# Performance work log

Measured on AMD Instinct MI355X. Metric: run time of the kernel, lower is better.

## Reference

```python
import jax, jax.numpy as jnp
import numpy as np

N_NODES = 100000
D_IN = 256
D_HID = 64
D_EMB = 32
ADJ_NNZ = 3200000
N_EDGES = 2000000


def setup_inputs() -> dict:
    key = jax.random.key(0)
    ks = jax.random.split(key, 8)
    x = jax.random.normal(ks[0], (N_NODES, D_IN), dtype=jnp.float32)
    adj_src = jax.random.randint(ks[1], (ADJ_NNZ,), 0, N_NODES, dtype=jnp.int32)
    adj_dst = jax.random.randint(ks[2], (ADJ_NNZ,), 0, N_NODES, dtype=jnp.int32)
    adj_val = jax.random.uniform(ks[3], (ADJ_NNZ,), dtype=jnp.float32)
    edge_index = jax.random.randint(ks[4], (2, N_EDGES), 0, N_NODES, dtype=jnp.int32)
    # Xavier-uniform weights, zero biases (matches reset_parameters)
    lim1 = float(np.sqrt(6.0 / (D_IN + D_HID)))
    lim2 = float(np.sqrt(6.0 / (D_HID + D_EMB)))
    W1 = jax.random.uniform(ks[5], (D_IN, D_HID), minval=-lim1, maxval=lim1, dtype=jnp.float32)
    b1 = jnp.zeros((D_HID,), dtype=jnp.float32)
    W2 = jax.random.uniform(ks[6], (D_HID, D_EMB), minval=-lim2, maxval=lim2, dtype=jnp.float32)
    b2 = jnp.zeros((D_EMB,), dtype=jnp.float32)
    return {"x": x, "adj_src": adj_src, "adj_dst": adj_dst, "adj_val": adj_val,
            "edge_index": edge_index, "W1": W1, "b1": b1, "W2": W2, "b2": b2}


def _spmm(adj_src, adj_dst, adj_val, dense):
    # (sparse A) @ dense : out[i] = sum_{e: dst[e]==i} val[e] * dense[src[e]]
    n = dense.shape[0]
    msgs = adj_val[:, None] * dense[adj_src]            # [nnz, d]
    return jax.ops.segment_sum(msgs, adj_dst, num_segments=n)


def reference(x, adj_src, adj_dst, adj_val, edge_index, W1, b1, W2, b2):
    # Layer 1: ReLU(A_norm @ (x W1) + b1)
    z1 = jax.nn.relu(_spmm(adj_src, adj_dst, adj_val, x @ W1) + b1)
    # Layer 2: A_norm @ (z1 W2) + b2 (no activation)
    z2 = _spmm(adj_src, adj_dst, adj_val, z1 @ W2) + b2   # [n, d_emb]
    # Inner-product decoder over edges
    src, dst = edge_index[0], edge_index[1]
    scores = jnp.sum(z2[src] * z2[dst], axis=1)          # [num_edges]
    return scores
```

## Files before the change

### kernel.cpp

```cpp
#include <hip/hip_runtime.h>
#include <hip/hip_bf16.h>


#define D_IN  256
#define D_HID 64
#define D_EMB 32
#define BROWS 256
#define NBUK_MAX 512
#define TILE  4096
#define PBS   512
#define SBS   1024

typedef unsigned char u8;
typedef unsigned short u16;
typedef unsigned int u32;
typedef __attribute__((ext_vector_type(8))) short short8;
typedef __attribute__((ext_vector_type(4))) float f32x4;
typedef __attribute__((ext_vector_type(2))) float f32x2;

__device__ __forceinline__ float bf2f(u32 u) {
  return __uint_as_float((u & 0xFFFFu) << 16);
}
__device__ __forceinline__ float bf2f_hi(u32 u) {
  return __uint_as_float(u & 0xFFFF0000u);
}
__device__ __forceinline__ u16 f2bf(float f) {
  u32 x = __float_as_uint(f);
  x += 0x7FFFu + ((x >> 16) & 1u);
  return (u16)(x >> 16);
}
__device__ __forceinline__ void unpack8(uint4 u, float* f) {
  f[0] = bf2f(u.x); f[1] = bf2f(u.x >> 16);
  f[2] = bf2f(u.y); f[3] = bf2f(u.y >> 16);
  f[4] = bf2f(u.z); f[5] = bf2f(u.z >> 16);
  f[6] = bf2f(u.w); f[7] = bf2f(u.w >> 16);
}

__global__ __launch_bounds__(256) void w1_swizzle_kernel(
    const float* __restrict__ W1, uint4* __restrict__ gswz) {
  const int s = blockIdx.x * 256 + threadIdx.x;
  const int lane = s & 63;
  const int kstep = (s >> 6) & 7;
  const int nt = s >> 9;
  const int col = nt * 16 + (lane & 15);
  const int kbase = kstep * 32 + (lane >> 4) * 8;
  u32 p[4];
  for (int jp = 0; jp < 4; ++jp) {
    u32 lo = f2bf(W1[(kbase + 2 * jp) * D_HID + col]);
    u32 hi = f2bf(W1[(kbase + 2 * jp + 1) * D_HID + col]);
    p[jp] = lo | (hi << 16);
  }
  gswz[s] = make_uint4(p[0], p[1], p[2], p[3]);
}

__global__ __launch_bounds__(256) void bin_count(
    const int* __restrict__ dst, int* __restrict__ hist, int nnz, int nbuk) {
  __shared__ int h[NBUK_MAX];
  for (int i = threadIdx.x; i < nbuk; i += 256) h[i] = 0;
  __syncthreads();
  const int stride = gridDim.x * 256;
  for (int e = blockIdx.x * 256 + threadIdx.x; e < nnz; e += stride)
    atomicAdd(&h[dst[e] >> 8], 1);
  __syncthreads();
  for (int i = threadIdx.x; i < nbuk; i += 256) {
    int v = h[i];
    if (v) atomicAdd(&hist[i], v);
  }
}

__global__ __launch_bounds__(256) void bin_scan(
    int* __restrict__ hist, int* __restrict__ cur, int n) {
  __shared__ int sm[256];
  const int t = threadIdx.x;
  const int per = (n + 255) / 256;
  const int base = t * per;
  int loc[4];
  int s = 0;
  for (int i = 0; i < per; ++i) {
    int idx = base + i;
    int v = (idx < n) ? hist[idx] : 0;
    loc[i] = s;
    s += v;
  }
  sm[t] = s;
  __syncthreads();
  for (int off = 1; off < 256; off <<= 1) {
    int tmp = (t >= off) ? sm[t - off] : 0;
    __syncthreads();
    sm[t] += tmp;
    __syncthreads();
  }
  const int b0 = sm[t] - s;
  for (int i = 0; i < per; ++i) {
    int idx = base + i;
    if (idx < n) {
      int p = b0 + loc[i];
      hist[idx] = p;
      cur[idx] = p;
    }
  }
  if (t == 255) hist[n] = sm[255];
}

__global__ __launch_bounds__(PBS) void partition_kernel(
    const int* __restrict__ src, const int* __restrict__ dst,
    const float* __restrict__ val, int* __restrict__ cur,
    int2* __restrict__ payload, int nnz, int nbuk) {
  __shared__ int2 stage[TILE];
  __shared__ int hist[NBUK_MAX];
  __shared__ int lcur[NBUK_MAX];
  __shared__ int gbase[NBUK_MAX];
  __shared__ int sm[PBS];

  const int t = threadIdx.x;
  const long long base = (long long)blockIdx.x * TILE;
  const int cnt = min(TILE, (int)(nnz - base));

  for (int i = t; i < nbuk; i += PBS) hist[i] = 0;
  __syncthreads();

  constexpr int PER = TILE / PBS;
  int key[PER], vq[PER];
  short bk[PER];
  for (int i = 0; i < PER; ++i) {
    int idx = t + i * PBS;
    if (idx < cnt) {
      int d = dst[base + idx];
      int b = d >> 8;
      bk[i] = (short)b;
      key[i] = (src[base + idx] << 8) | (d & (BROWS - 1));
      int q = (int)(val[base + idx] * 32768.f + 0.5f);
      q = min(q, 32767);
      vq[i] = (b << 15) | q;
      atomicAdd(&hist[b], 1);
    } else {
      bk[i] = -1;
    }
  }
  __syncthreads();

  {
    int c = (t < nbuk) ? hist[t] : 0;
    sm[t] = c;
    __syncthreads();
    for (int off = 1; off < PBS; off <<= 1) {
      int tmp = (t >= off) ? sm[t - off] : 0;
      __syncthreads();
      sm[t] += tmp;
      __syncthreads();
    }
    int excl = sm[t] - c;
    if (t < nbuk) {
      hist[t] = excl;
      lcur[t] = excl;
      if (c > 0) gbase[t] = atomicAdd(&cur[t], c);
    }
  }
  __syncthreads();

  for (int i = 0; i < PER; ++i) {
    if (bk[i] >= 0) {
      int p = atomicAdd(&lcur[bk[i]], 1);
      stage[p] = make_int2(key[i], vq[i]);
    }
  }
  __syncthreads();

  for (int i = t; i < cnt; i += PBS) {
    int2 pk = stage[i];
    int b = pk.y >> 15;
    payload[gbase[b] + (i - hist[b])] = pk;
  }
}

__global__ __launch_bounds__(SBS) void bucket_sort_kernel(
    const int* __restrict__ bscan, const int2* __restrict__ payload,
    u32* __restrict__ csr, int* __restrict__ rs, int M) {
  __shared__ int cnt_s[BROWS * 4];
  __shared__ int sm[BROWS * 4];
  const int b = blockIdx.x;
  const int t = threadIdx.x;
  const int start = bscan[b];
  const int end = bscan[b + 1];

  cnt_s[t] = 0;
  __syncthreads();
  for (int j = start + t; j < end; j += SBS) {
    int k = payload[j].x;
    int bin = ((k & (BROWS - 1)) << 2) | ((k >> 23) & 3);
    atomicAdd(&cnt_s[bin], 1);
  }
  __syncthreads();

  int v = cnt_s[t];
  sm[t] = v;
  __syncthreads();
  for (int off = 1; off < SBS; off <<= 1) {
    int tmp = (t >= off) ? sm[t - off] : 0;
    __syncthreads();
    sm[t] += tmp;
    __syncthreads();
  }
  if ((t & 3) == 3) {
    int row = b * BROWS + (t >> 2);
    if (row < M) rs[row] = start + sm[t];
  }
  cnt_s[t] = start + sm[t] - v;
  __syncthreads();

  for (int j = start + t; j < end; j += SBS) {
    int2 pk = payload[j];
    int bin = ((pk.x & (BROWS - 1)) << 2) | ((pk.x >> 23) & 3);
    int p = atomicAdd(&cnt_s[bin], 1);
    csr[p] = ((u32)(pk.x >> 8) << 15) | (u32)(pk.y & 32767);
  }
}

__global__ __launch_bounds__(256) void gemm1_mfma_kernel(
    const float* __restrict__ x, const uint4* __restrict__ gswz,
    u8* __restrict__ h1, int M) {
  const int tid = threadIdx.x;
  const int wv = tid >> 6;
  const int lane = tid & 63;
  const int quad = lane >> 4;
  const int m = lane & 15;

  const int rowbase = blockIdx.x * 64 + wv * 16;
  int arow = rowbase + m;
  if (arow >= M) arow = M - 1;

  f32x4 acc[4];
  for (int nt = 0; nt < 4; ++nt) acc[nt] = (f32x4){0.f, 0.f, 0.f, 0.f};

  const float* xrow = &x[(long long)arow * D_IN];

#pragma unroll
  for (int kstep = 0; kstep < 8; ++kstep) {
    const int kbase = kstep * 32 + quad * 8;
    float4 a0 = *(const float4*)&xrow[kbase];
    float4 a1 = *(const float4*)&xrow[kbase + 4];
    short8 af;
    af[0] = (short)f2bf(a0.x); af[1] = (short)f2bf(a0.y);
    af[2] = (short)f2bf(a0.z); af[3] = (short)f2bf(a0.w);
    af[4] = (short)f2bf(a1.x); af[5] = (short)f2bf(a1.y);
    af[6] = (short)f2bf(a1.z); af[7] = (short)f2bf(a1.w);
#pragma unroll
    for (int nt = 0; nt < 4; ++nt) {
      uint4 bu = gswz[(nt * 8 + kstep) * 64 + lane];
      short8 bf = *(short8*)&bu;
      acc[nt] = __builtin_amdgcn_mfma_f32_16x16x32_bf16(af, bf, acc[nt], 0, 0, 0);
    }
  }

#pragma unroll
  for (int nt = 0; nt < 4; ++nt) {
#pragma unroll
    for (int r = 0; r < 4; ++r) {
      int orow = rowbase + quad * 4 + r;
      if (orow < M) {
        int pk8 = __builtin_amdgcn_cvt_pk_fp8_f32(acc[nt][r], 0.f, 0, false);
        h1[(u32)orow * D_HID + nt * 16 + m] = (u8)(pk8 & 0xFF);
      }
    }
  }
}

__global__ __launch_bounds__(256) void spmm1_gemm2_fused(
    const int* __restrict__ rs, const u32* __restrict__ csr,
    const u8* __restrict__ in, const float* __restrict__ b1,
    const float* __restrict__ W2, u16* __restrict__ h2, int M) {
  __shared__ float w2s[D_HID * D_EMB];
  __shared__ float z1s[16][68];

  const int tid = threadIdx.x;
  for (int i = tid; i < D_HID * D_EMB / 4; i += 256)
    ((float4*)w2s)[i] = ((const float4*)W2)[i];
  __syncthreads();

  const int lt = tid & 15;
  const int tb = tid >> 4;
  const int row = blockIdx.x * 16 + tb;
  if (row >= M) return;

  const int start = (row == 0) ? 0 : rs[row - 1];
  const int end = rs[row];
  const float qs = 1.f / 32768.f;
  const u8* inp = in + lt * 4;

  float a0 = 0.f, a1 = 0.f, a2 = 0.f, a3 = 0.f;
  int j = start;

#define GATHER_FMA(PK)                                                \
  {                                                                   \
    u32 wq = *(const u32*)(inp + (((PK) >> 15) << 6));                \
    float v = (float)((PK) & 32767u) * qs;                            \
    f32x2 lo = __builtin_amdgcn_cvt_pk_f32_fp8(wq, false);            \
    f32x2 hi = __builtin_amdgcn_cvt_pk_f32_fp8(wq, true);             \
    a0 = fmaf(v, lo.x, a0); a1 = fmaf(v, lo.y, a1);                   \
    a2 = fmaf(v, hi.x, a2); a3 = fmaf(v, hi.y, a3);                   \
  }

  int head = (4 - (start & 3)) & 3;
  if (head > end - start) head = end - start;
  for (int h = 0; h < head; ++h, ++j) {
    u32 pk = csr[j];
    GATHER_FMA(pk);
  }

  for (; j + 8 <= end; j += 8) {
    uint4 pa = *(const uint4*)&csr[j];
    uint4 pb = *(const uint4*)&csr[j + 4];
    u32 w0 = *(const u32*)(inp + ((pa.x >> 15) << 6));
    u32 w1 = *(const u32*)(inp + ((pa.y >> 15) << 6));
    u32 w2 = *(const u32*)(inp + ((pa.z >> 15) << 6));
    u32 w3 = *(const u32*)(inp + ((pa.w >> 15) << 6));
    u32 w4 = *(const u32*)(inp + ((pb.x >> 15) << 6));
    u32 w5 = *(const u32*)(inp + ((pb.y >> 15) << 6));
    u32 w6 = *(const u32*)(inp + ((pb.z >> 15) << 6));
    u32 w7 = *(const u32*)(inp + ((pb.w >> 15) << 6));
    float v0 = (float)(pa.x & 32767u) * qs;
    float v1 = (float)(pa.y & 32767u) * qs;
    float v2 = (float)(pa.z & 32767u) * qs;
    float v3 = (float)(pa.w & 32767u) * qs;
    float v4 = (float)(pb.x & 32767u) * qs;
    float v5 = (float)(pb.y & 32767u) * qs;
    float v6 = (float)(pb.z & 32767u) * qs;
    float v7 = (float)(pb.w & 32767u) * qs;
    f32x2 l0 = __builtin_amdgcn_cvt_pk_f32_fp8(w0, false);
    f32x2 h0 = __builtin_amdgcn_cvt_pk_f32_fp8(w0, true);
    f32x2 l1 = __builtin_amdgcn_cvt_pk_f32_fp8(w1, false);
    f32x2 h1f = __builtin_amdgcn_cvt_pk_f32_fp8(w1, true);
    f32x2 l2 = __builtin_amdgcn_cvt_pk_f32_fp8(w2, false);
    f32x2 h2f = __builtin_amdgcn_cvt_pk_f32_fp8(w2, true);
    f32x2 l3 = __builtin_amdgcn_cvt_pk_f32_fp8(w3, false);
    f32x2 h3 = __builtin_amdgcn_cvt_pk_f32_fp8(w3, true);
    f32x2 l4 = __builtin_amdgcn_cvt_pk_f32_fp8(w4, false);
    f32x2 h4 = __builtin_amdgcn_cvt_pk_f32_fp8(w4, true);
    f32x2 l5 = __builtin_amdgcn_cvt_pk_f32_fp8(w5, false);
    f32x2 h5 = __builtin_amdgcn_cvt_pk_f32_fp8(w5, true);
    f32x2 l6 = __builtin_amdgcn_cvt_pk_f32_fp8(w6, false);
    f32x2 h6 = __builtin_amdgcn_cvt_pk_f32_fp8(w6, true);
    f32x2 l7 = __builtin_amdgcn_cvt_pk_f32_fp8(w7, false);
    f32x2 h7 = __builtin_amdgcn_cvt_pk_f32_fp8(w7, true);
    a0 = fmaf(v0, l0.x, a0); a1 = fmaf(v0, l0.y, a1);
    a2 = fmaf(v0, h0.x, a2); a3 = fmaf(v0, h0.y, a3);
    a0 = fmaf(v1, l1.x, a0); a1 = fmaf(v1, l1.y, a1);
    a2 = fmaf(v1, h1f.x, a2); a3 = fmaf(v1, h1f.y, a3);
    a0 = fmaf(v2, l2.x, a0); a1 = fmaf(v2, l2.y, a1);
    a2 = fmaf(v2, h2f.x, a2); a3 = fmaf(v2, h2f.y, a3);
    a0 = fmaf(v3, l3.x, a0); a1 = fmaf(v3, l3.y, a1);
    a2 = fmaf(v3, h3.x, a2); a3 = fmaf(v3, h3.y, a3);
    a0 = fmaf(v4, l4.x, a0); a1 = fmaf(v4, l4.y, a1);
    a2 = fmaf(v4, h4.x, a2); a3 = fmaf(v4, h4.y, a3);
    a0 = fmaf(v5, l5.x, a0); a1 = fmaf(v5, l5.y, a1);
    a2 = fmaf(v5, h5.x, a2); a3 = fmaf(v5, h5.y, a3);
    a0 = fmaf(v6, l6.x, a0); a1 = fmaf(v6, l6.y, a1);
    a2 = fmaf(v6, h6.x, a2); a3 = fmaf(v6, h6.y, a3);
    a0 = fmaf(v7, l7.x, a0); a1 = fmaf(v7, l7.y, a1);
    a2 = fmaf(v7, h7.x, a2); a3 = fmaf(v7, h7.y, a3);
  }

  for (; j < end; ++j) {
    u32 pk = csr[j];
    GATHER_FMA(pk);
  }
#undef GATHER_FMA

  const float4 bv = *(const float4*)&b1[lt * 4];
  a0 = fmaxf(a0 + bv.x, 0.f);
  a1 = fmaxf(a1 + bv.y, 0.f);
  a2 = fmaxf(a2 + bv.z, 0.f);
  a3 = fmaxf(a3 + bv.w, 0.f);

  float* zrow = z1s[tb];
  zrow[lt * 4 + 0] = a0;
  zrow[lt * 4 + 1] = a1;
  zrow[lt * 4 + 2] = a2;
  zrow[lt * 4 + 3] = a3;
  float o0 = 0.f, o1 = 0.f;
#pragma unroll
  for (int k = 0; k < D_HID; k += 4) {
    float4 z4 = *(const float4*)&zrow[k];
    o0 = fmaf(z4.x, w2s[(k + 0) * D_EMB + 2 * lt], o0);
    o1 = fmaf(z4.x, w2s[(k + 0) * D_EMB + 2 * lt + 1], o1);
    o0 = fmaf(z4.y, w2s[(k + 1) * D_EMB + 2 * lt], o0);
    o1 = fmaf(z4.y, w2s[(k + 1) * D_EMB + 2 * lt + 1], o1);
    o0 = fmaf(z4.z, w2s[(k + 2) * D_EMB + 2 * lt], o0);
    o1 = fmaf(z4.z, w2s[(k + 2) * D_EMB + 2 * lt + 1], o1);
    o0 = fmaf(z4.w, w2s[(k + 3) * D_EMB + 2 * lt], o0);
    o1 = fmaf(z4.w, w2s[(k + 3) * D_EMB + 2 * lt + 1], o1);
  }
  u32 o = (u32)f2bf(o0) | ((u32)f2bf(o1) << 16);
  ((u32*)h2)[((u32)row << 4) + lt] = o;
}

template <int D, bool RELU>
__global__ __launch_bounds__(256) void spmm_csr_kernel(
    const int* __restrict__ rs, const u32* __restrict__ csr,
    const u16* __restrict__ in, const float* __restrict__ bias,
    u16* __restrict__ out, int M) {
  constexpr int TEAM = D / 4;
  constexpr int SH = (D == 64) ? 6 : 5;
  const int lt = threadIdx.x % TEAM;
  const int row = blockIdx.x * (256 / TEAM) + threadIdx.x / TEAM;
  if (row >= M) return;
  const int start = (row == 0) ? 0 : rs[row - 1];
  const int end = rs[row];
  const float qs = 1.f / 32768.f;
  const u16* inp = in + lt * 4;

  float a0 = 0.f, a1 = 0.f, a2 = 0.f, a3 = 0.f;
  int j = start;

  int head = (4 - (start & 3)) & 3;
  if (head > end - start) head = end - start;
  for (int h = 0; h < head; ++h, ++j) {
    u32 pk = csr[j];
    uint2 w = *(const uint2*)(inp + ((pk >> 15) << SH));
    float v = (float)(pk & 32767u) * qs;
    a0 = fmaf(v, bf2f(w.x), a0); a1 = fmaf(v, bf2f_hi(w.x), a1);
    a2 = fmaf(v, bf2f(w.y), a2); a3 = fmaf(v, bf2f_hi(w.y), a3);
  }

  for (; j + 8 <= end; j += 8) {
    uint4 pa = *(const uint4*)&csr[j];
    uint4 pb = *(const uint4*)&csr[j + 4];
    uint2 w0 = *(const uint2*)(inp + ((pa.x >> 15) << SH));
    uint2 w1 = *(const uint2*)(inp + ((pa.y >> 15) << SH));
    uint2 w2 = *(const uint2*)(inp + ((pa.z >> 15) << SH));
    uint2 w3 = *(const uint2*)(inp + ((pa.w >> 15) << SH));
    uint2 w4 = *(const uint2*)(inp + ((pb.x >> 15) << SH));
    uint2 w5 = *(const uint2*)(inp + ((pb.y >> 15) << SH));
    uint2 w6 = *(const uint2*)(inp + ((pb.z >> 15) << SH));
    uint2 w7 = *(const uint2*)(inp + ((pb.w >> 15) << SH));
    float v0 = (float)(pa.x & 32767u) * qs;
    float v1 = (float)(pa.y & 32767u) * qs;
    float v2 = (float)(pa.z & 32767u) * qs;
    float v3 = (float)(pa.w & 32767u) * qs;
    float v4 = (float)(pb.x & 32767u) * qs;
    float v5 = (float)(pb.y & 32767u) * qs;
    float v6 = (float)(pb.z & 32767u) * qs;
    float v7 = (float)(pb.w & 32767u) * qs;
    a0 = fmaf(v0, bf2f(w0.x), a0); a1 = fmaf(v0, bf2f_hi(w0.x), a1);
    a2 = fmaf(v0, bf2f(w0.y), a2); a3 = fmaf(v0, bf2f_hi(w0.y), a3);
    a0 = fmaf(v1, bf2f(w1.x), a0); a1 = fmaf(v1, bf2f_hi(w1.x), a1);
    a2 = fmaf(v1, bf2f(w1.y), a2); a3 = fmaf(v1, bf2f_hi(w1.y), a3);
    a0 = fmaf(v2, bf2f(w2.x), a0); a1 = fmaf(v2, bf2f_hi(w2.x), a1);
    a2 = fmaf(v2, bf2f(w2.y), a2); a3 = fmaf(v2, bf2f_hi(w2.y), a3);
    a0 = fmaf(v3, bf2f(w3.x), a0); a1 = fmaf(v3, bf2f_hi(w3.x), a1);
    a2 = fmaf(v3, bf2f(w3.y), a2); a3 = fmaf(v3, bf2f_hi(w3.y), a3);
    a0 = fmaf(v4, bf2f(w4.x), a0); a1 = fmaf(v4, bf2f_hi(w4.x), a1);
    a2 = fmaf(v4, bf2f(w4.y), a2); a3 = fmaf(v4, bf2f_hi(w4.y), a3);
    a0 = fmaf(v5, bf2f(w5.x), a0); a1 = fmaf(v5, bf2f_hi(w5.x), a1);
    a2 = fmaf(v5, bf2f(w5.y), a2); a3 = fmaf(v5, bf2f_hi(w5.y), a3);
    a0 = fmaf(v6, bf2f(w6.x), a0); a1 = fmaf(v6, bf2f_hi(w6.x), a1);
    a2 = fmaf(v6, bf2f(w6.y), a2); a3 = fmaf(v6, bf2f_hi(w6.y), a3);
    a0 = fmaf(v7, bf2f(w7.x), a0); a1 = fmaf(v7, bf2f_hi(w7.x), a1);
    a2 = fmaf(v7, bf2f(w7.y), a2); a3 = fmaf(v7, bf2f_hi(w7.y), a3);
  }

  for (; j + 4 <= end; j += 4) {
    uint4 p = *(const uint4*)&csr[j];
    uint2 w0 = *(const uint2*)(inp + ((p.x >> 15) << SH));
    uint2 w1 = *(const uint2*)(inp + ((p.y >> 15) << SH));
    uint2 w2 = *(const uint2*)(inp + ((p.z >> 15) << SH));
    uint2 w3 = *(const uint2*)(inp + ((p.w >> 15) << SH));
    float v0 = (float)(p.x & 32767u) * qs;
    float v1 = (float)(p.y & 32767u) * qs;
    float v2 = (float)(p.z & 32767u) * qs;
    float v3 = (float)(p.w & 32767u) * qs;
    a0 = fmaf(v0, bf2f(w0.x), a0); a1 = fmaf(v0, bf2f_hi(w0.x), a1);
    a2 = fmaf(v0, bf2f(w0.y), a2); a3 = fmaf(v0, bf2f_hi(w0.y), a3);
    a0 = fmaf(v1, bf2f(w1.x), a0); a1 = fmaf(v1, bf2f_hi(w1.x), a1);
    a2 = fmaf(v1, bf2f(w1.y), a2); a3 = fmaf(v1, bf2f_hi(w1.y), a3);
    a0 = fmaf(v2, bf2f(w2.x), a0); a1 = fmaf(v2, bf2f_hi(w2.x), a1);
    a2 = fmaf(v2, bf2f(w2.y), a2); a3 = fmaf(v2, bf2f_hi(w2.y), a3);
    a0 = fmaf(v3, bf2f(w3.x), a0); a1 = fmaf(v3, bf2f_hi(w3.x), a1);
    a2 = fmaf(v3, bf2f(w3.y), a2); a3 = fmaf(v3, bf2f_hi(w3.y), a3);
  }
  for (; j < end; ++j) {
    u32 pk = csr[j];
    uint2 w = *(const uint2*)(inp + ((pk >> 15) << SH));
    float v = (float)(pk & 32767u) * qs;
    a0 = fmaf(v, bf2f(w.x), a0); a1 = fmaf(v, bf2f_hi(w.x), a1);
    a2 = fmaf(v, bf2f(w.y), a2); a3 = fmaf(v, bf2f_hi(w.y), a3);
  }
  const float4 bv = *(const float4*)&bias[lt * 4];
  a0 += bv.x; a1 += bv.y; a2 += bv.z; a3 += bv.w;
  if (RELU) {
    a0 = fmaxf(a0, 0.f); a1 = fmaxf(a1, 0.f);
    a2 = fmaxf(a2, 0.f); a3 = fmaxf(a3, 0.f);
  }
  uint2 o;
  o.x = (u32)f2bf(a0) | ((u32)f2bf(a1) << 16);
  o.y = (u32)f2bf(a2) | ((u32)f2bf(a3) << 16);
  *(uint2*)&out[((u32)row << SH) + lt * 4] = o;
}

__global__ __launch_bounds__(256) void decode_kernel(
    const int* __restrict__ ei, const u16* __restrict__ z2,
    float* __restrict__ out, int nE) {
  const int t = blockIdx.x * 256 + threadIdx.x;
  const int e0 = t * 2;
  if (e0 >= nE) return;
  const bool two = (e0 + 1 < nE);

  const int2 ss = *(const int2*)&ei[e0];
  const int2 dd = *(const int2*)&ei[nE + e0];

  const uint4* za = (const uint4*)(z2 + ((u32)ss.x << 5));
  const uint4* zb = (const uint4*)(z2 + ((u32)dd.x << 5));
  const uint4* zc = (const uint4*)(z2 + ((u32)(two ? ss.y : ss.x) << 5));
  const uint4* zd = (const uint4*)(z2 + ((u32)(two ? dd.y : dd.x) << 5));

  uint4 A[2], B[2], C[2], Dv[2];
  A[0] = za[0]; A[1] = za[1];
  B[0] = zb[0]; B[1] = zb[1];
  C[0] = zc[0]; C[1] = zc[1];
  Dv[0] = zd[0]; Dv[1] = zd[1];
  uint4 A2[2], B2[2], C2[2], D2[2];
  A2[0] = za[2]; A2[1] = za[3];
  B2[0] = zb[2]; B2[1] = zb[3];
  C2[0] = zc[2]; C2[1] = zc[3];
  D2[0] = zd[2]; D2[1] = zd[3];

  float acc0 = 0.f, acc1 = 0.f;
  float a8[8], b8[8];
#pragma unroll
  for (int c = 0; c < 2; ++c) {
    unpack8(A[c], a8); unpack8(B[c], b8);
#pragma unroll
    for (int k = 0; k < 8; ++k) acc0 = fmaf(a8[k], b8[k], acc0);
    unpack8(A2[c], a8); unpack8(B2[c], b8);
#pragma unroll
    for (int k = 0; k < 8; ++k) acc0 = fmaf(a8[k], b8[k], acc0);
    unpack8(C[c], a8); unpack8(Dv[c], b8);
#pragma unroll
    for (int k = 0; k < 8; ++k) acc1 = fmaf(a8[k], b8[k], acc1);
    unpack8(C2[c], a8); unpack8(D2[c], b8);
#pragma unroll
    for (int k = 0; k < 8; ++k) acc1 = fmaf(a8[k], b8[k], acc1);
  }
  out[e0] = acc0;
  if (two) out[e0 + 1] = acc1;
}

extern "C" void kernel_launch(void* const* d_in, const int* in_sizes, int n_in,
                              void* d_out, int out_size, void* d_ws, size_t ws_size,
                              hipStream_t stream) {
  const float* x       = (const float*)d_in[0];
  const int*   adj_src = (const int*)d_in[1];
  const int*   adj_dst = (const int*)d_in[2];
  const float* adj_val = (const float*)d_in[3];
  const int*   ei      = (const int*)d_in[4];
  const float* W1      = (const float*)d_in[5];
  const float* b1      = (const float*)d_in[6];
  const float* W2      = (const float*)d_in[7];
  const float* b2      = (const float*)d_in[8];

  const int M   = in_sizes[0] / D_IN;
  const int nnz = in_sizes[1];
  const int nE  = in_sizes[4] / 2;

  const int NBUK = (M + BROWS - 1) / BROWS;

  char* ws = (char*)d_ws;
  u32*   csr     = (u32*)(ws);
  int2*  payload = (int2*)(ws + (size_t)nnz * 4);
  u8*    h1      = (u8*)(ws + (size_t)nnz * 4);
  u16*   h2      = (u16*)(ws + (size_t)nnz * 4 + (size_t)M * D_HID);
  u16*   z2      = (u16*)(ws + (size_t)nnz * 12);
  uint4* gswz    = (uint4*)(ws + 60ull * 1024 * 1024);

  int* rs    = (int*)d_out;
  int* bscan = (int*)d_out + 112 * 1024;
  int* cur   = (int*)d_out + 120 * 1024;

  w1_swizzle_kernel<<<8, 256, 0, stream>>>(W1, gswz);

  hipMemsetAsync(bscan, 0, (size_t)(NBUK + 1) * 4, stream);
  bin_count<<<256, 256, 0, stream>>>(adj_dst, bscan, nnz, NBUK);
  bin_scan<<<1, 256, 0, stream>>>(bscan, cur, NBUK);
  partition_kernel<<<(nnz + TILE - 1) / TILE, PBS, 0, stream>>>(
      adj_src, adj_dst, adj_val, cur, payload, nnz, NBUK);

  bucket_sort_kernel<<<NBUK, SBS, 0, stream>>>(bscan, payload, csr, rs, M);

  gemm1_mfma_kernel<<<(M + 63) / 64, 256, 0, stream>>>(x, gswz, h1, M);

  spmm1_gemm2_fused<<<(M + 15) / 16, 256, 0, stream>>>(
      rs, csr, h1, b1, W2, h2, M);

  spmm_csr_kernel<D_EMB, false><<<(M + 31) / 32, 256, 0, stream>>>(
      rs, csr, h2, b2, z2, M);

  decode_kernel<<<(nE / 2 + 255) / 256, 256, 0, stream>>>(ei, z2, (float*)d_out, nE);
}
```

Measured before the change: 415.3 us.

## Simplify bucket sort bins, use hardware bf16 pack converts, relocate h1/h2 buffers

The bucket sort drops its four sub-bins per row, which were keyed on a high bit field of the key, and now bins only by row. This shrinks the shared histogram and the scan from 1024 to 256 entries, but changes the order of entries within each CSR row. Manual round-to-nearest bf16 conversions are replaced with the v_cvt_pk_bf16_f32 instruction in the GEMM1, W2 projection and SpMM epilogues. The h1/h2 buffers move to fixed workspace offsets, so they no longer alias the payload region and may stop sharing cache-resident memory.

Result: no change. 418.3 us (+0.7%).

```diff
diff --git a/kernel.cpp b/kernel.cpp
--- a/kernel.cpp
+++ b/kernel.cpp
@@ -28,6 +28,11 @@
   u32 x = __float_as_uint(f);
   x += 0x7FFFu + ((x >> 16) & 1u);
   return (u16)(x >> 16);
+}
+__device__ __forceinline__ u32 cvtpk_bf16(float lo, float hi) {
+  u32 r;
+  asm("v_cvt_pk_bf16_f32 %0, %1, %2" : "=v"(r) : "v"(lo), "v"(hi));
+  return r;
 }
 __device__ __forceinline__ void unpack8(uint4 u, float* f) {
   f[0] = bf2f(u.x); f[1] = bf2f(u.x >> 16);
@@ -176,42 +181,40 @@
 __global__ __launch_bounds__(SBS) void bucket_sort_kernel(
     const int* __restrict__ bscan, const int2* __restrict__ payload,
     u32* __restrict__ csr, int* __restrict__ rs, int M) {
-  __shared__ int cnt_s[BROWS * 4];
-  __shared__ int sm[BROWS * 4];
+  __shared__ int cnt_s[BROWS];
+  __shared__ int sm[BROWS];
   const int b = blockIdx.x;
   const int t = threadIdx.x;
   const int start = bscan[b];
   const int end = bscan[b + 1];
 
-  cnt_s[t] = 0;
-  __syncthreads();
-  for (int j = start + t; j < end; j += SBS) {
-    int k = payload[j].x;
-    int bin = ((k & (BROWS - 1)) << 2) | ((k >> 23) & 3);
-    atomicAdd(&cnt_s[bin], 1);
-  }
-  __syncthreads();
-
-  int v = cnt_s[t];
-  sm[t] = v;
-  __syncthreads();
-  for (int off = 1; off < SBS; off <<= 1) {
-    int tmp = (t >= off) ? sm[t - off] : 0;
+  if (t < BROWS) cnt_s[t] = 0;
+  __syncthreads();
+  for (int j = start + t; j < end; j += SBS)
+    atomicAdd(&cnt_s[payload[j].x & (BROWS - 1)], 1);
+  __syncthreads();
+
+  int v = 0;
+  if (t < BROWS) { v = cnt_s[t]; sm[t] = v; }
+  __syncthreads();
+  for (int off = 1; off < BROWS; off <<= 1) {
+    int tmp = 0;
+    if (t < BROWS && t >= off) tmp = sm[t - off];
     __syncthreads();
-    sm[t] += tmp;
+    if (t < BROWS) sm[t] += tmp;
     __syncthreads();
   }
-  if ((t & 3) == 3) {
-    int row = b * BROWS + (t >> 2);
+  if (t < BROWS) {
+    int row = b * BROWS + t;
     if (row < M) rs[row] = start + sm[t];
-  }
-  cnt_s[t] = start + sm[t] - v;
+    cnt_s[t] = start + sm[t] - v;
+  }
   __syncthreads();
 
   for (int j = start + t; j < end; j += SBS) {
     int2 pk = payload[j];
-    int bin = ((pk.x & (BROWS - 1)) << 2) | ((pk.x >> 23) & 3);
-    int p = atomicAdd(&cnt_s[bin], 1);
+    int r = pk.x & (BROWS - 1);
+    int p = atomicAdd(&cnt_s[r], 1);
     csr[p] = ((u32)(pk.x >> 8) << 15) | (u32)(pk.y & 32767);
   }
 }
@@ -239,11 +242,12 @@
     const int kbase = kstep * 32 + quad * 8;
     float4 a0 = *(const float4*)&xrow[kbase];
     float4 a1 = *(const float4*)&xrow[kbase + 4];
-    short8 af;
-    af[0] = (short)f2bf(a0.x); af[1] = (short)f2bf(a0.y);
-    af[2] = (short)f2bf(a0.z); af[3] = (short)f2bf(a0.w);
-    af[4] = (short)f2bf(a1.x); af[5] = (short)f2bf(a1.y);
-    af[6] = (short)f2bf(a1.z); af[7] = (short)f2bf(a1.w);
+    uint4 au;
+    au.x = cvtpk_bf16(a0.x, a0.y);
+    au.y = cvtpk_bf16(a0.z, a0.w);
+    au.z = cvtpk_bf16(a1.x, a1.y);
+    au.w = cvtpk_bf16(a1.z, a1.w);
+    short8 af = *(short8*)&au;
 #pragma unroll
     for (int nt = 0; nt < 4; ++nt) {
       uint4 bu = gswz[(nt * 8 + kstep) * 64 + lane];
@@ -390,8 +394,7 @@
     o0 = fmaf(z4.w, w2s[(k + 3) * D_EMB + 2 * lt], o0);
     o1 = fmaf(z4.w, w2s[(k + 3) * D_EMB + 2 * lt + 1], o1);
   }
-  u32 o = (u32)f2bf(o0) | ((u32)f2bf(o1) << 16);
-  ((u32*)h2)[((u32)row << 4) + lt] = o;
+  ((u32*)h2)[((u32)row << 4) + lt] = cvtpk_bf16(o0, o1);
 }
 
 template <int D, bool RELU>
@@ -492,8 +495,8 @@
     a2 = fmaxf(a2, 0.f); a3 = fmaxf(a3, 0.f);
   }
   uint2 o;
-  o.x = (u32)f2bf(a0) | ((u32)f2bf(a1) << 16);
-  o.y = (u32)f2bf(a2) | ((u32)f2bf(a3) << 16);
+  o.x = cvtpk_bf16(a0, a1);
+  o.y = cvtpk_bf16(a2, a3);
   *(uint2*)&out[((u32)row << SH) + lt * 4] = o;
 }
 
@@ -567,9 +570,9 @@
   char* ws = (char*)d_ws;
   u32*   csr     = (u32*)(ws);
   int2*  payload = (int2*)(ws + (size_t)nnz * 4);
-  u8*    h1      = (u8*)(ws + (size_t)nnz * 4);
-  u16*   h2      = (u16*)(ws + (size_t)nnz * 4 + (size_t)M * D_HID);
   u16*   z2      = (u16*)(ws + (size_t)nnz * 12);
+  u8*    h1      = (u8*)(ws + 44800ull * 1024);
+  u16*   h2      = (u16*)(ws + 51200ull * 1024);
   uint4* gswz    = (uint4*)(ws + 60ull * 1024 * 1024);
 
   int* rs    = (int*)d_out;
```
